# Performance work log

Measured on AMD Instinct MI355X. Metric: run time of the kernel, lower is better.

## Reference

```python
import jax, jax.numpy as jnp
import numpy as np

G = 2048        # number of graphs in the batch
TURNS = 6       # debate turns (fixed in source)
NPT = 48        # nodes per (graph, turn) segment
NHID = 128      # config.nhid; mode != 'bidirection' -> nlast = nhid
BN_EPS = 1e-5


def setup_inputs() -> dict:
    key = jax.random.key(0)
    k1, k2, k3 = jax.random.split(key, 3)
    N = G * TURNS * NPT
    hp = jax.random.normal(k1, (N, NHID), dtype=jnp.float32)
    idx = jnp.arange(N, dtype=jnp.int32)
    graph_ids = idx // (TURNS * NPT)          # [N] graph membership
    turn_ids = (idx // NPT) % TURNS           # [N] 'ids' node attribute (turn)
    # xavier_normal_ init as in the source
    W1 = jax.random.normal(k2, (NHID // 2, 2 * NHID), dtype=jnp.float32) * np.sqrt(2.0 / (NHID // 2 + 2 * NHID)).astype(np.float32)
    b1 = jnp.zeros((NHID // 2,), dtype=jnp.float32)
    W4 = jax.random.normal(k3, (1, NHID // 2), dtype=jnp.float32) * np.sqrt(2.0 / (1 + NHID // 2)).astype(np.float32)
    b4 = jnp.zeros((1,), dtype=jnp.float32)
    return {
        "hp": hp, "graph_ids": graph_ids, "turn_ids": turn_ids,
        "W1": W1, "b1": b1, "W4": W4, "b4": b4,
        "bn1_gamma": jnp.ones((1,), jnp.float32), "bn1_beta": jnp.zeros((1,), jnp.float32),
        "bn2_gamma": jnp.ones((1,), jnp.float32), "bn2_beta": jnp.zeros((1,), jnp.float32),
    }


def _bn_eval(x, gamma, beta):
    # BatchNorm1d(1) in eval mode: running_mean=0, running_var=1, single channel
    return x * (gamma / jnp.sqrt(1.0 + BN_EPS)) + beta


def reference(hp, graph_ids, turn_ids, W1, b1, W4, b4,
              bn1_gamma, bn1_beta, bn2_gamma, bn2_beta):
    # fused segment readout keyed on (graph, turn) -- replaces the
    # per-graph per-turn unbatch/filter_nodes Python loops
    seg = graph_ids * TURNS + turn_ids                       # [N]
    nseg = G * TURNS
    hmax = jax.ops.segment_max(hp, seg, num_segments=nseg).reshape(G, TURNS, NHID)
    hmin = jax.ops.segment_min(hp, seg, num_segments=nseg).reshape(G, TURNS, NHID)
    # _read_out_loud(op='max') accumulates even turns into s1,
    # _read_out_loud(op='min') accumulates odd turns into s2
    x1 = hmax[:, 0::2, :].sum(axis=1)                        # [G, NHID]
    x2 = hmin[:, 1::2, :].sum(axis=1)                        # [G, NHID]
    x = jnp.concatenate([x1, x2], axis=-1)[:, None, :]       # [G, 1, 2*NHID]
    # MLP head (eval mode: dropout is identity)
    x = _bn_eval(x, bn1_gamma, bn1_beta)
    y = jax.nn.relu(jnp.einsum('gcl,hl->gch', x, W1) + b1)   # [G, 1, NHID//2]
    y = _bn_eval(y, bn2_gamma, bn2_beta)
    out = jnp.einsum('gch,oh->gco', y, W4) + b4              # [G, 1, 1]
    return out.squeeze()                                     # [G]
```

## Files before the change

### kernel.cpp

```cpp
#include <hip/hip_runtime.h>

#define NGRAPH 2048
#define TURNS  6
#define NPT    48
#define NHID   128
#define NC4    (NHID / 4)
#define BN_EPS 1e-5f

__device__ __forceinline__ float4 f4max(float4 a, float4 b) {
    return make_float4(fmaxf(a.x, b.x), fmaxf(a.y, b.y), fmaxf(a.z, b.z), fmaxf(a.w, b.w));
}
__device__ __forceinline__ float4 f4min(float4 a, float4 b) {
    return make_float4(fminf(a.x, b.x), fminf(a.y, b.y), fminf(a.z, b.z), fminf(a.w, b.w));
}
__device__ __forceinline__ float4 f4add(float4 a, float4 b) {
    return make_float4(a.x + b.x, a.y + b.y, a.z + b.z, a.w + b.w);
}

__global__ __launch_bounds__(192) void ggru_readout_mlp(
    const float* __restrict__ hp,
    const float* __restrict__ W1, const float* __restrict__ b1,
    const float* __restrict__ W4, const float* __restrict__ b4,
    const float* __restrict__ bn1_g, const float* __restrict__ bn1_b,
    const float* __restrict__ bn2_g, const float* __restrict__ bn2_b,
    float* __restrict__ out)
{
    __shared__ float4 segres[TURNS][NC4];
    __shared__ float  xbn[2 * NHID];

    const int g    = blockIdx.x;
    const int tid  = threadIdx.x;
    const int col  = tid & 31;
    const int turn = tid >> 5;

    const float4* rowbase = reinterpret_cast<const float4*>(hp)
                          + (size_t)(g * TURNS + turn) * NPT * NC4 + col;

    float4 acc = rowbase[0];
    if ((turn & 1) == 0) {
        #pragma unroll 4
        for (int r = 1; r < NPT; ++r)
            acc = f4max(acc, rowbase[r * NC4]);
    } else {
        #pragma unroll 4
        for (int r = 1; r < NPT; ++r)
            acc = f4min(acc, rowbase[r * NC4]);
    }
    segres[turn][col] = acc;
    __syncthreads();

    if (tid < 64) {
        float4 s;
        if (tid < 32) {
            s = f4add(f4add(segres[0][tid], segres[2][tid]), segres[4][tid]);
        } else {
            int c = tid - 32;
            s = f4add(f4add(segres[1][c], segres[3][c]), segres[5][c]);
        }
        const float s1 = bn1_g[0] / sqrtf(1.0f + BN_EPS);
        const float t1 = bn1_b[0];
        s.x = s.x * s1 + t1;
        s.y = s.y * s1 + t1;
        s.z = s.z * s1 + t1;
        s.w = s.w * s1 + t1;
        reinterpret_cast<float4*>(xbn)[tid] = s;
    }
    __syncthreads();

    if (tid < 64) {
        float acc2 = b1[tid];
        const float4* w  = reinterpret_cast<const float4*>(W1 + tid * (2 * NHID));
        const float4* xv = reinterpret_cast<const float4*>(xbn);
        #pragma unroll 8
        for (int k = 0; k < (2 * NHID) / 4; ++k) {
            const float4 wv = w[k];
            const float4 x  = xv[k];
            acc2 += wv.x * x.x + wv.y * x.y + wv.z * x.z + wv.w * x.w;
        }
        float y = fmaxf(acc2, 0.0f);
        const float s2 = bn2_g[0] / sqrtf(1.0f + BN_EPS);
        y = y * s2 + bn2_b[0];

        float p = y * W4[tid];
        #pragma unroll
        for (int off = 32; off > 0; off >>= 1)
            p += __shfl_down(p, off, 64);
        if (tid == 0)
            out[g] = p + b4[0];
    }
}

extern "C" void kernel_launch(void* const* d_in, const int* in_sizes, int n_in,
                              void* d_out, int out_size, void* d_ws, size_t ws_size,
                              hipStream_t stream) {
    (void)in_sizes; (void)n_in; (void)d_ws; (void)ws_size; (void)out_size;
    const float* hp    = (const float*)d_in[0];
    const float* W1    = (const float*)d_in[3];
    const float* b1    = (const float*)d_in[4];
    const float* W4    = (const float*)d_in[5];
    const float* b4    = (const float*)d_in[6];
    const float* bn1_g = (const float*)d_in[7];
    const float* bn1_b = (const float*)d_in[8];
    const float* bn2_g = (const float*)d_in[9];
    const float* bn2_b = (const float*)d_in[10];
    float* out = (float*)d_out;

    hipLaunchKernelGGL(ggru_readout_mlp, dim3(NGRAPH), dim3(192), 0, stream,
                       hp, W1, b1, W4, b4, bn1_g, bn1_b, bn2_g, bn2_b, out);
}
```

Before: 63.72 us.

## Split each segment's row reduction across two thread halves and use nontemporal loads

Doubles the block to 384 threads so each (turn, column) reduction covers half of the 48 rows. The two partial max/min results are combined in shared memory before the turn sums. Streaming loads of hp now use nontemporal hints to avoid polluting the cache. This shortens the serial dependent load chain per thread and adds memory-level parallelism, at the cost of more threads per block and an extra combine step.

Measured after the change: 58.95 us. 1.08x faster.

```diff
diff --git a/kernel.cpp b/kernel.cpp
--- a/kernel.cpp
+++ b/kernel.cpp
@@ -7,17 +7,22 @@
 #define NC4    (NHID / 4)
 #define BN_EPS 1e-5f
 
-__device__ __forceinline__ float4 f4max(float4 a, float4 b) {
-    return make_float4(fmaxf(a.x, b.x), fmaxf(a.y, b.y), fmaxf(a.z, b.z), fmaxf(a.w, b.w));
+typedef float f32x4 __attribute__((ext_vector_type(4)));
+
+__device__ __forceinline__ f32x4 f4max(f32x4 a, f32x4 b) {
+    f32x4 r;
+    r.x = fmaxf(a.x, b.x); r.y = fmaxf(a.y, b.y);
+    r.z = fmaxf(a.z, b.z); r.w = fmaxf(a.w, b.w);
+    return r;
 }
-__device__ __forceinline__ float4 f4min(float4 a, float4 b) {
-    return make_float4(fminf(a.x, b.x), fminf(a.y, b.y), fminf(a.z, b.z), fminf(a.w, b.w));
-}
-__device__ __forceinline__ float4 f4add(float4 a, float4 b) {
-    return make_float4(a.x + b.x, a.y + b.y, a.z + b.z, a.w + b.w);
+__device__ __forceinline__ f32x4 f4min(f32x4 a, f32x4 b) {
+    f32x4 r;
+    r.x = fminf(a.x, b.x); r.y = fminf(a.y, b.y);
+    r.z = fminf(a.z, b.z); r.w = fminf(a.w, b.w);
+    return r;
 }
 
-__global__ __launch_bounds__(192) void ggru_readout_mlp(
+__global__ __launch_bounds__(384) void ggru_readout_mlp(
     const float* __restrict__ hp,
     const float* __restrict__ W1, const float* __restrict__ b1,
     const float* __restrict__ W4, const float* __restrict__ b4,
@@ -25,56 +30,63 @@
     const float* __restrict__ bn2_g, const float* __restrict__ bn2_b,
     float* __restrict__ out)
 {
-    __shared__ float4 segres[TURNS][NC4];
-    __shared__ float  xbn[2 * NHID];
+    __shared__ f32x4 segres[2][TURNS][NC4];
+    __shared__ float xbn[2 * NHID];
 
     const int g    = blockIdx.x;
     const int tid  = threadIdx.x;
     const int col  = tid & 31;
-    const int turn = tid >> 5;
+    const int tt   = tid >> 5;
+    const int half = (tt >= TURNS) ? 1 : 0;
+    const int turn = tt - TURNS * half;
 
-    const float4* rowbase = reinterpret_cast<const float4*>(hp)
-                          + (size_t)(g * TURNS + turn) * NPT * NC4 + col;
+    const f32x4* rowbase = reinterpret_cast<const f32x4*>(hp)
+                         + ((size_t)(g * TURNS + turn) * NPT + half * (NPT / 2)) * NC4
+                         + col;
 
-    float4 acc = rowbase[0];
+    f32x4 acc = __builtin_nontemporal_load(&rowbase[0]);
     if ((turn & 1) == 0) {
-        #pragma unroll 4
-        for (int r = 1; r < NPT; ++r)
-            acc = f4max(acc, rowbase[r * NC4]);
+        #pragma unroll 8
+        for (int r = 1; r < NPT / 2; ++r)
+            acc = f4max(acc, __builtin_nontemporal_load(&rowbase[r * NC4]));
     } else {
-        #pragma unroll 4
-        for (int r = 1; r < NPT; ++r)
-            acc = f4min(acc, rowbase[r * NC4]);
+        #pragma unroll 8
+        for (int r = 1; r < NPT / 2; ++r)
+            acc = f4min(acc, __builtin_nontemporal_load(&rowbase[r * NC4]));
     }
-    segres[turn][col] = acc;
+    segres[half][turn][col] = acc;
     __syncthreads();
 
     if (tid < 64) {
-        float4 s;
+        const int c = tid & 31;
+        f32x4 s;
         if (tid < 32) {
-            s = f4add(f4add(segres[0][tid], segres[2][tid]), segres[4][tid]);
+            f32x4 t0 = f4max(segres[0][0][c], segres[1][0][c]);
+            f32x4 t2 = f4max(segres[0][2][c], segres[1][2][c]);
+            f32x4 t4 = f4max(segres[0][4][c], segres[1][4][c]);
+            s = t0 + t2 + t4;
         } else {
-            int c = tid - 32;
-            s = f4add(f4add(segres[1][c], segres[3][c]), segres[5][c]);
+            f32x4 t1 = f4min(segres[0][1][c], segres[1][1][c]);
+            f32x4 t3 = f4min(segres[0][3][c], segres[1][3][c]);
+            f32x4 t5 = f4min(segres[0][5][c], segres[1][5][c]);
+            s = t1 + t3 + t5;
         }
         const float s1 = bn1_g[0] / sqrtf(1.0f + BN_EPS);
         const float t1 = bn1_b[0];
-        s.x = s.x * s1 + t1;
-        s.y = s.y * s1 + t1;
-        s.z = s.z * s1 + t1;
-        s.w = s.w * s1 + t1;
-        reinterpret_cast<float4*>(xbn)[tid] = s;
+        s = s * s1;
+        s.x += t1; s.y += t1; s.z += t1; s.w += t1;
+        reinterpret_cast<f32x4*>(xbn)[tid] = s;
     }
     __syncthreads();
 
     if (tid < 64) {
         float acc2 = b1[tid];
-        const float4* w  = reinterpret_cast<const float4*>(W1 + tid * (2 * NHID));
-        const float4* xv = reinterpret_cast<const float4*>(xbn);
+        const f32x4* w  = reinterpret_cast<const f32x4*>(W1 + tid * (2 * NHID));
+        const f32x4* xv = reinterpret_cast<const f32x4*>(xbn);
         #pragma unroll 8
         for (int k = 0; k < (2 * NHID) / 4; ++k) {
-            const float4 wv = w[k];
-            const float4 x  = xv[k];
+            const f32x4 wv = w[k];
+            const f32x4 x  = xv[k];
             acc2 += wv.x * x.x + wv.y * x.y + wv.z * x.z + wv.w * x.w;
         }
         float y = fmaxf(acc2, 0.0f);
@@ -105,6 +117,6 @@
     const float* bn2_b = (const float*)d_in[10];
     float* out = (float*)d_out;
 
-    hipLaunchKernelGGL(ggru_readout_mlp, dim3(NGRAPH), dim3(192), 0, stream,
+    hipLaunchKernelGGL(ggru_readout_mlp, dim3(NGRAPH), dim3(384), 0, stream,
                        hp, W1, b1, W4, b4, bn1_g, bn1_b, bn2_g, bn2_b, out);
 }
```
